# Performance work log

Hardware: AMD Instinct MI355X
Metric: run time of the kernel (lower is better)

## Reference

```python
import jax, jax.numpy as jnp
import numpy as np

N = 50000
E = 1600000
F_IN = 128
F_OUT = 64
NEG_SLOPE = 0.2


def setup_inputs() -> dict:
    key = jax.random.key(0)
    k1, k2, k3, k4, k5, k6 = jax.random.split(key, 6)
    x = jax.random.normal(k1, (N, F_IN), dtype=jnp.float32)
    edge_index = jax.random.randint(k2, (2, E), 0, N, dtype=jnp.int64)
    # GATConv params (heads=1): glorot-ish scale
    W = jax.random.normal(k3, (F_IN, F_OUT), dtype=jnp.float32) * (1.0 / np.sqrt(F_IN))
    att_src = jax.random.normal(k4, (F_OUT,), dtype=jnp.float32) * (1.0 / np.sqrt(F_OUT))
    att_dst = jax.random.normal(k5, (F_OUT,), dtype=jnp.float32) * (1.0 / np.sqrt(F_OUT))
    bias = jnp.zeros((F_OUT,), dtype=jnp.float32)
    return {"x": x, "edge_index": edge_index, "W": W, "att_src": att_src, "att_dst": att_dst, "bias": bias}


def _gat_forward(x, edge_index, W, att_src, att_dst, bias):
    n = x.shape[0]
    # add self loops (PyG GATConv default)
    loops = jnp.arange(n, dtype=edge_index.dtype)
    src = jnp.concatenate([edge_index[0], loops])  # [E+N]
    dst = jnp.concatenate([edge_index[1], loops])  # [E+N]

    h = x @ W                                      # [N, F_OUT]
    a_src = h @ att_src                            # [N]
    a_dst = h @ att_dst                            # [N]

    e = a_src[src] + a_dst[dst]                    # [E+N]
    e = jnp.where(e > 0, e, NEG_SLOPE * e)         # LeakyReLU(0.2)

    # softmax over edges grouped by destination node
    e_max = jax.ops.segment_max(e, dst, num_segments=n)     # [N]
    e_exp = jnp.exp(e - e_max[dst])                          # [E+N]
    e_sum = jax.ops.segment_sum(e_exp, dst, num_segments=n)  # [N]
    alpha = e_exp / e_sum[dst]                               # [E+N]

    msg = h[src] * alpha[:, None]                            # [E+N, F_OUT]
    out = jax.ops.segment_sum(msg, dst, num_segments=n)      # [N, F_OUT]
    out = out + bias
    return jax.nn.relu(out)


def reference(x, edge_index, W, att_src, att_dst, bias):
    return _gat_forward(x, edge_index, W, att_src, att_dst, bias)
```

## Files before the change

kernel.cpp:

```cpp
#include <hip/hip_runtime.h>

#define NN 50000
#define NE 1600000
#define NE4 400000
#define FIN 128
#define FOUT 64
#define SLOPE 0.2f

#define NPB  16
#define NBF  3125
#define CAPB 768
#define GBLK 782
#define CHC4 512
#define LW   136

typedef unsigned int u32;
typedef short short8 __attribute__((ext_vector_type(8)));
typedef float f32x4 __attribute__((ext_vector_type(4)));

__device__ __forceinline__ unsigned short f2bf(float f) {
    u32 u = __float_as_uint(f);
    u += 0x7FFFu + ((u >> 16) & 1u);
    return (unsigned short)(u >> 16);
}
__device__ __forceinline__ float bf2f(unsigned short s) {
    return __uint_as_float(((u32)s) << 16);
}

union FusedLds {
    unsigned short Wt[64 * LW];
    struct { int cnt[NBF]; int gb[NBF]; } f;
};

__global__ __launch_bounds__(256) void fused_k(
        const float* __restrict__ x, const float* __restrict__ W,
        const float* __restrict__ att_s, const float* __restrict__ att_d,
        const int* __restrict__ ei, int* __restrict__ fcur,
        u32* __restrict__ fstage, unsigned short* __restrict__ h,
        float* __restrict__ a_src, float* __restrict__ a_dst) {
    __shared__ FusedLds L;
    const int tid = threadIdx.x;

    {
        unsigned short* Wt = L.Wt;
        const int node0 = blockIdx.x * 64;
        for (int i = tid; i < 128 * 16; i += 256) {
            int k = i >> 4, f = (i & 15) * 4;
            float4 w4 = ((const float4*)W)[i];
            Wt[(f + 0) * LW + k] = f2bf(w4.x);
            Wt[(f + 1) * LW + k] = f2bf(w4.y);
            Wt[(f + 2) * LW + k] = f2bf(w4.z);
            Wt[(f + 3) * LW + k] = f2bf(w4.w);
        }
        const int wv = tid >> 6, lane = tid & 63;
        const int q = lane >> 4, mr = lane & 15;
        const int row = node0 + wv * 16 + mr;
        const bool valid = row < NN;
        const float4* x4 = (const float4*)x;

        short8 afr[4];
        #pragma unroll
        for (int ks = 0; ks < 4; ++ks) {
            float4 f0 = make_float4(0.f, 0.f, 0.f, 0.f), f1 = f0;
            if (valid) {
                f0 = x4[(size_t)row * 32 + ks * 8 + q * 2];
                f1 = x4[(size_t)row * 32 + ks * 8 + q * 2 + 1];
            }
            short8 a;
            a[0] = (short)f2bf(f0.x); a[1] = (short)f2bf(f0.y);
            a[2] = (short)f2bf(f0.z); a[3] = (short)f2bf(f0.w);
            a[4] = (short)f2bf(f1.x); a[5] = (short)f2bf(f1.y);
            a[6] = (short)f2bf(f1.z); a[7] = (short)f2bf(f1.w);
            afr[ks] = a;
        }
        __syncthreads();

        f32x4 acc[4] = {{0,0,0,0},{0,0,0,0},{0,0,0,0},{0,0,0,0}};
        #pragma unroll
        for (int ks = 0; ks < 4; ++ks) {
            #pragma unroll
            for (int nt = 0; nt < 4; ++nt) {
                short8 b = *(const short8*)(Wt + (nt * 16 + mr) * LW + ks * 32 + q * 8);
                acc[nt] = __builtin_amdgcn_mfma_f32_16x16x32_bf16(afr[ks], b, acc[nt], 0, 0, 0);
            }
        }
        float atts[4], attd[4];
        #pragma unroll
        for (int nt = 0; nt < 4; ++nt) {
            atts[nt] = att_s[nt * 16 + mr];
            attd[nt] = att_d[nt * 16 + mr];
        }
        #pragma unroll
        for (int r = 0; r < 4; ++r) {
            int node = node0 + wv * 16 + q * 4 + r;
            float ps = 0.f, pd = 0.f;
            #pragma unroll
            for (int nt = 0; nt < 4; ++nt) {
                float v = acc[nt][r];
                if (node < NN) h[(size_t)node * 64 + nt * 16 + mr] = f2bf(v);
                ps += v * atts[nt];
                pd += v * attd[nt];
            }
            #pragma unroll
            for (int off = 8; off > 0; off >>= 1) {
                ps += __shfl_xor(ps, off);
                pd += __shfl_xor(pd, off);
            }
            if (mr == 0 && node < NN) { a_src[node] = ps; a_dst[node] = pd; }
        }
    }
    __syncthreads();

    for (int i = tid; i < NBF; i += 256) L.f.cnt[i] = 0;
    __syncthreads();

    const int4* sd4 = (const int4*)(ei + NE);
    const int4* ss4 = (const int4*)ei;
    const int lo = blockIdx.x * CHC4;
    int bkx[2][4];
    u32 payx[2][4];
    #pragma unroll
    for (int u = 0; u < 2; ++u) {
        const int i = lo + tid + u * 256;
        if (i < NE4) {
            int4 d = sd4[i];
            int4 s = ss4[i];
            bkx[u][0] = d.x >> 4; payx[u][0] = (u32)s.x | ((u32)(d.x & 15) << 16);
            bkx[u][1] = d.y >> 4; payx[u][1] = (u32)s.y | ((u32)(d.y & 15) << 16);
            bkx[u][2] = d.z >> 4; payx[u][2] = (u32)s.z | ((u32)(d.z & 15) << 16);
            bkx[u][3] = d.w >> 4; payx[u][3] = (u32)s.w | ((u32)(d.w & 15) << 16);
            atomicAdd(&L.f.cnt[bkx[u][0]], 1);
            atomicAdd(&L.f.cnt[bkx[u][1]], 1);
            atomicAdd(&L.f.cnt[bkx[u][2]], 1);
            atomicAdd(&L.f.cnt[bkx[u][3]], 1);
        } else {
            bkx[u][0] = bkx[u][1] = bkx[u][2] = bkx[u][3] = -1;
        }
    }
    __syncthreads();
    for (int b = tid; b < NBF; b += 256) {
        int tot = L.f.cnt[b];
        L.f.gb[b] = tot ? atomicAdd(&fcur[b], tot) : 0;
        L.f.cnt[b] = 0;
    }
    __syncthreads();
    #pragma unroll
    for (int u = 0; u < 2; ++u) {
        #pragma unroll
        for (int e = 0; e < 4; ++e) {
            int b = bkx[u][e];
            if (b >= 0) {
                int pos = L.f.gb[b] + atomicAdd(&L.f.cnt[b], 1);
                if (pos < CAPB) fstage[(size_t)b * CAPB + pos] = payx[u][e];
            }
        }
    }
}

__global__ __launch_bounds__(256) void agg_k(
        const u32* __restrict__ staging, const int* __restrict__ bcur,
        const float* __restrict__ a_src, const float* __restrict__ a_dst,
        const ushort4* __restrict__ h4, const float* __restrict__ bias,
        float* __restrict__ out) {
    const int bkt = blockIdx.x;
    const int node0 = bkt << 4;
    const int nNodes = min(NPB, NN - node0);
    const int bsize = min(bcur[bkt], CAPB);
    const u32* stg = staging + (size_t)bkt * CAPB;
    const int tid = threadIdx.x, wv = tid >> 6, lane = tid & 63;

    __shared__ u32 pk[CAPB];
    __shared__ unsigned short ssrc[CAPB];
    __shared__ int lcnt[NPB];
    __shared__ int lbase[NPB + 1];
    __shared__ int lcur[NPB];
    float* evals = (float*)pk;

    for (int j = tid; j < bsize; j += 256) pk[j] = stg[j];
    if (tid < NPB) lcnt[tid] = 0;
    __syncthreads();
    for (int j = tid; j < bsize; j += 256)
        atomicAdd(&lcnt[pk[j] >> 16], 1);
    __syncthreads();
    if (tid < 64) {
        int v = (tid < NPB) ? lcnt[tid] : 0;
        #pragma unroll
        for (int off = 1; off < NPB; off <<= 1) {
            int u = __shfl_up(v, off);
            if (tid >= off) v += u;
        }
        if (tid < NPB) lbase[tid + 1] = v;
        if (tid == 0) lbase[0] = 0;
    }
    if (tid >= 64 && tid < 64 + NPB) lcur[tid - 64] = 0;
    __syncthreads();
    for (int j = tid; j < bsize; j += 256) {
        u32 w = pk[j];
        int ld = w >> 16;
        int pos = lbase[ld] + atomicAdd(&lcur[ld], 1);
        ssrc[pos] = (unsigned short)(w & 0xFFFFu);
    }
    __syncthreads();

    const int q = lane >> 4, ql = lane & 15;
    const float4 b4 = ((const float4*)bias)[ql];
    const int ln = wv * 4 + q;
    if (ln >= nNodes) return;
    const int n = node0 + ln;
    const int st = lbase[ln], deg = lbase[ln + 1] - st;
    const float ad = a_dst[n];
    float es = a_src[n] + ad; es = es > 0.f ? es : SLOPE * es;
    const float ps = __expf(es);
    float sum = 0.f;
    for (int j = ql; j < deg; j += 16) {
        int s = ssrc[st + j];
        float e = a_src[s] + ad; e = e > 0.f ? e : SLOPE * e;
        float pe = __expf(e);
        evals[st + j] = pe;
        sum += pe;
    }
    sum += __shfl_xor(sum, 8); sum += __shfl_xor(sum, 4);
    sum += __shfl_xor(sum, 2); sum += __shfl_xor(sum, 1);
    const float inv = 1.f / (sum + ps);

    ushort4 hs = h4[(size_t)n * 16 + ql];
    float a0 = ps * bf2f(hs.x), a1 = ps * bf2f(hs.y);
    float a2 = ps * bf2f(hs.z), a3 = ps * bf2f(hs.w);
    int j = 0;
    for (; j + 4 <= deg; j += 4) {
        int s0 = ssrc[st + j], s1 = ssrc[st + j + 1];
        int s2 = ssrc[st + j + 2], s3 = ssrc[st + j + 3];
        float e0 = evals[st + j], e1 = evals[st + j + 1];
        float e2 = evals[st + j + 2], e3 = evals[st + j + 3];
        ushort4 v0 = h4[(size_t)s0 * 16 + ql];
        ushort4 v1 = h4[(size_t)s1 * 16 + ql];
        ushort4 v2 = h4[(size_t)s2 * 16 + ql];
        ushort4 v3 = h4[(size_t)s3 * 16 + ql];
        a0 += e0 * bf2f(v0.x); a1 += e0 * bf2f(v0.y);
        a2 += e0 * bf2f(v0.z); a3 += e0 * bf2f(v0.w);
        a0 += e1 * bf2f(v1.x); a1 += e1 * bf2f(v1.y);
        a2 += e1 * bf2f(v1.z); a3 += e1 * bf2f(v1.w);
        a0 += e2 * bf2f(v2.x); a1 += e2 * bf2f(v2.y);
        a2 += e2 * bf2f(v2.z); a3 += e2 * bf2f(v2.w);
        a0 += e3 * bf2f(v3.x); a1 += e3 * bf2f(v3.y);
        a2 += e3 * bf2f(v3.z); a3 += e3 * bf2f(v3.w);
    }
    for (; j < deg; ++j) {
        int s = ssrc[st + j];
        float ev = evals[st + j];
        ushort4 hv = h4[(size_t)s * 16 + ql];
        a0 += ev * bf2f(hv.x); a1 += ev * bf2f(hv.y);
        a2 += ev * bf2f(hv.z); a3 += ev * bf2f(hv.w);
    }
    float4 o;
    o.x = a0 * inv + b4.x; o.x = o.x > 0.f ? o.x : 0.f;
    o.y = a1 * inv + b4.y; o.y = o.y > 0.f ? o.y : 0.f;
    o.z = a2 * inv + b4.z; o.z = o.z > 0.f ? o.z : 0.f;
    o.w = a3 * inv + b4.w; o.w = o.w > 0.f ? o.w : 0.f;
    ((float4*)out)[(size_t)n * 16 + ql] = o;
}

extern "C" void kernel_launch(void* const* d_in, const int* in_sizes, int n_in,
                              void* d_out, int out_size, void* d_ws, size_t ws_size,
                              hipStream_t stream) {
    const float* x     = (const float*)d_in[0];
    const int*   ei    = (const int*)d_in[1];
    const float* W     = (const float*)d_in[2];
    const float* att_s = (const float*)d_in[3];
    const float* att_d = (const float*)d_in[4];
    const float* bias  = (const float*)d_in[5];
    float* out = (float*)d_out;

    unsigned short* h = (unsigned short*)d_ws;
    float* a_src  = (float*)(h + (size_t)NN * 64);
    float* a_dst  = a_src + NN;
    int*   fcur   = (int*)(a_dst + NN);
    u32*   fstage = (u32*)(fcur + 3200);

    hipMemsetAsync(fcur, 0, NBF * sizeof(int), stream);

    fused_k<<<GBLK, 256, 0, stream>>>(x, W, att_s, att_d, ei, fcur,
                                      fstage, h, a_src, a_dst);
    agg_k<<<NBF, 256, 0, stream>>>(fstage, fcur, a_src, a_dst,
                                   (const ushort4*)h, bias, out);
}
```

Baseline: 169.2 us.

## Coarsen destination buckets to 128 nodes with 1024-thread aggregation blocks

Changes edge binning from 16-node buckets to 128-node buckets, cutting bucket count from 3125 to 391, and runs the aggregation with 1024-thread blocks in which each 16-lane group handles two nodes. The aim is fewer global atomics and smaller LDS counter arrays in the binning pass, and lower block scheduling overhead. The local scan becomes a two-wave scan with a fix-up step. In exchange, aggregation has far fewer blocks, which risks poorer load balance and less latency hiding across CUs.

```diff
diff --git a/kernel.cpp b/kernel.cpp
--- a/kernel.cpp
+++ b/kernel.cpp
@@ -7,9 +7,9 @@
 #define FOUT 64
 #define SLOPE 0.2f
 
-#define NPB  16
-#define NBF  3125
-#define CAPB 768
+#define NPB  128
+#define NBC  391
+#define CAPB 4800
 #define GBLK 782
 #define CHC4 512
 #define LW   136
@@ -29,7 +29,7 @@
 
 union FusedLds {
     unsigned short Wt[64 * LW];
-    struct { int cnt[NBF]; int gb[NBF]; } f;
+    struct { int cnt[NBC]; int gb[NBC]; } f;
 };
 
 __global__ __launch_bounds__(256) void fused_k(
@@ -111,7 +111,7 @@
     }
     __syncthreads();
 
-    for (int i = tid; i < NBF; i += 256) L.f.cnt[i] = 0;
+    for (int i = tid; i < NBC; i += 256) L.f.cnt[i] = 0;
     __syncthreads();
 
     const int4* sd4 = (const int4*)(ei + NE);
@@ -125,10 +125,10 @@
         if (i < NE4) {
             int4 d = sd4[i];
             int4 s = ss4[i];
-            bkx[u][0] = d.x >> 4; payx[u][0] = (u32)s.x | ((u32)(d.x & 15) << 16);
-            bkx[u][1] = d.y >> 4; payx[u][1] = (u32)s.y | ((u32)(d.y & 15) << 16);
-            bkx[u][2] = d.z >> 4; payx[u][2] = (u32)s.z | ((u32)(d.z & 15) << 16);
-            bkx[u][3] = d.w >> 4; payx[u][3] = (u32)s.w | ((u32)(d.w & 15) << 16);
+            bkx[u][0] = d.x >> 7; payx[u][0] = (u32)s.x | ((u32)(d.x & 127) << 16);
+            bkx[u][1] = d.y >> 7; payx[u][1] = (u32)s.y | ((u32)(d.y & 127) << 16);
+            bkx[u][2] = d.z >> 7; payx[u][2] = (u32)s.z | ((u32)(d.z & 127) << 16);
+            bkx[u][3] = d.w >> 7; payx[u][3] = (u32)s.w | ((u32)(d.w & 127) << 16);
             atomicAdd(&L.f.cnt[bkx[u][0]], 1);
             atomicAdd(&L.f.cnt[bkx[u][1]], 1);
             atomicAdd(&L.f.cnt[bkx[u][2]], 1);
@@ -138,7 +138,7 @@
         }
     }
     __syncthreads();
-    for (int b = tid; b < NBF; b += 256) {
+    for (int b = tid; b < NBC; b += 256) {
         int tot = L.f.cnt[b];
         L.f.gb[b] = tot ? atomicAdd(&fcur[b], tot) : 0;
         L.f.cnt[b] = 0;
@@ -157,13 +157,13 @@
     }
 }
 
-__global__ __launch_bounds__(256) void agg_k(
+__global__ __launch_bounds__(1024) void agg_k(
         const u32* __restrict__ staging, const int* __restrict__ bcur,
         const float* __restrict__ a_src, const float* __restrict__ a_dst,
         const ushort4* __restrict__ h4, const float* __restrict__ bias,
         float* __restrict__ out) {
     const int bkt = blockIdx.x;
-    const int node0 = bkt << 4;
+    const int node0 = bkt << 7;
     const int nNodes = min(NPB, NN - node0);
     const int bsize = min(bcur[bkt], CAPB);
     const u32* stg = staging + (size_t)bkt * CAPB;
@@ -176,25 +176,28 @@
     __shared__ int lcur[NPB];
     float* evals = (float*)pk;
 
-    for (int j = tid; j < bsize; j += 256) pk[j] = stg[j];
+    for (int j = tid; j < bsize; j += 1024) pk[j] = stg[j];
     if (tid < NPB) lcnt[tid] = 0;
     __syncthreads();
-    for (int j = tid; j < bsize; j += 256)
+    for (int j = tid; j < bsize; j += 1024)
         atomicAdd(&lcnt[pk[j] >> 16], 1);
     __syncthreads();
-    if (tid < 64) {
-        int v = (tid < NPB) ? lcnt[tid] : 0;
-        #pragma unroll
-        for (int off = 1; off < NPB; off <<= 1) {
+    if (tid < 128) {
+        int l = tid & 63;
+        int v = lcnt[tid];
+        #pragma unroll
+        for (int off = 1; off < 64; off <<= 1) {
             int u = __shfl_up(v, off);
-            if (tid >= off) v += u;
-        }
-        if (tid < NPB) lbase[tid + 1] = v;
+            if (l >= off) v += u;
+        }
+        lbase[tid + 1] = v;
         if (tid == 0) lbase[0] = 0;
     }
-    if (tid >= 64 && tid < 64 + NPB) lcur[tid - 64] = 0;
-    __syncthreads();
-    for (int j = tid; j < bsize; j += 256) {
+    if (tid >= 128 && tid < 256) lcur[tid - 128] = 0;
+    __syncthreads();
+    if (tid >= 64 && tid < 128) lbase[tid + 1] += lbase[64];
+    __syncthreads();
+    for (int j = tid; j < bsize; j += 1024) {
         u32 w = pk[j];
         int ld = w >> 16;
         int pos = lbase[ld] + atomicAdd(&lcur[ld], 1);
@@ -204,60 +207,64 @@
 
     const int q = lane >> 4, ql = lane & 15;
     const float4 b4 = ((const float4*)bias)[ql];
-    const int ln = wv * 4 + q;
-    if (ln >= nNodes) return;
-    const int n = node0 + ln;
-    const int st = lbase[ln], deg = lbase[ln + 1] - st;
-    const float ad = a_dst[n];
-    float es = a_src[n] + ad; es = es > 0.f ? es : SLOPE * es;
-    const float ps = __expf(es);
-    float sum = 0.f;
-    for (int j = ql; j < deg; j += 16) {
-        int s = ssrc[st + j];
-        float e = a_src[s] + ad; e = e > 0.f ? e : SLOPE * e;
-        float pe = __expf(e);
-        evals[st + j] = pe;
-        sum += pe;
-    }
-    sum += __shfl_xor(sum, 8); sum += __shfl_xor(sum, 4);
-    sum += __shfl_xor(sum, 2); sum += __shfl_xor(sum, 1);
-    const float inv = 1.f / (sum + ps);
-
-    ushort4 hs = h4[(size_t)n * 16 + ql];
-    float a0 = ps * bf2f(hs.x), a1 = ps * bf2f(hs.y);
-    float a2 = ps * bf2f(hs.z), a3 = ps * bf2f(hs.w);
-    int j = 0;
-    for (; j + 4 <= deg; j += 4) {
-        int s0 = ssrc[st + j], s1 = ssrc[st + j + 1];
-        int s2 = ssrc[st + j + 2], s3 = ssrc[st + j + 3];
-        float e0 = evals[st + j], e1 = evals[st + j + 1];
-        float e2 = evals[st + j + 2], e3 = evals[st + j + 3];
-        ushort4 v0 = h4[(size_t)s0 * 16 + ql];
-        ushort4 v1 = h4[(size_t)s1 * 16 + ql];
-        ushort4 v2 = h4[(size_t)s2 * 16 + ql];
-        ushort4 v3 = h4[(size_t)s3 * 16 + ql];
-        a0 += e0 * bf2f(v0.x); a1 += e0 * bf2f(v0.y);
-        a2 += e0 * bf2f(v0.z); a3 += e0 * bf2f(v0.w);
-        a0 += e1 * bf2f(v1.x); a1 += e1 * bf2f(v1.y);
-        a2 += e1 * bf2f(v1.z); a3 += e1 * bf2f(v1.w);
-        a0 += e2 * bf2f(v2.x); a1 += e2 * bf2f(v2.y);
-        a2 += e2 * bf2f(v2.z); a3 += e2 * bf2f(v2.w);
-        a0 += e3 * bf2f(v3.x); a1 += e3 * bf2f(v3.y);
-        a2 += e3 * bf2f(v3.z); a3 += e3 * bf2f(v3.w);
-    }
-    for (; j < deg; ++j) {
-        int s = ssrc[st + j];
-        float ev = evals[st + j];
-        ushort4 hv = h4[(size_t)s * 16 + ql];
-        a0 += ev * bf2f(hv.x); a1 += ev * bf2f(hv.y);
-        a2 += ev * bf2f(hv.z); a3 += ev * bf2f(hv.w);
-    }
-    float4 o;
-    o.x = a0 * inv + b4.x; o.x = o.x > 0.f ? o.x : 0.f;
-    o.y = a1 * inv + b4.y; o.y = o.y > 0.f ? o.y : 0.f;
-    o.z = a2 * inv + b4.z; o.z = o.z > 0.f ? o.z : 0.f;
-    o.w = a3 * inv + b4.w; o.w = o.w > 0.f ? o.w : 0.f;
-    ((float4*)out)[(size_t)n * 16 + ql] = o;
+    const int quad = wv * 4 + q;
+    #pragma unroll
+    for (int t = 0; t < 2; ++t) {
+        const int ln = quad * 2 + t;
+        if (ln >= nNodes) continue;
+        const int n = node0 + ln;
+        const int st = lbase[ln], deg = lbase[ln + 1] - st;
+        const float ad = a_dst[n];
+        float es = a_src[n] + ad; es = es > 0.f ? es : SLOPE * es;
+        const float ps = __expf(es);
+        float sum = 0.f;
+        for (int j = ql; j < deg; j += 16) {
+            int s = ssrc[st + j];
+            float e = a_src[s] + ad; e = e > 0.f ? e : SLOPE * e;
+            float pe = __expf(e);
+            evals[st + j] = pe;
+            sum += pe;
+        }
+        sum += __shfl_xor(sum, 8); sum += __shfl_xor(sum, 4);
+        sum += __shfl_xor(sum, 2); sum += __shfl_xor(sum, 1);
+        const float inv = 1.f / (sum + ps);
+
+        ushort4 hs = h4[(size_t)n * 16 + ql];
+        float a0 = ps * bf2f(hs.x), a1 = ps * bf2f(hs.y);
+        float a2 = ps * bf2f(hs.z), a3 = ps * bf2f(hs.w);
+        int j = 0;
+        for (; j + 4 <= deg; j += 4) {
+            int s0 = ssrc[st + j], s1 = ssrc[st + j + 1];
+            int s2 = ssrc[st + j + 2], s3 = ssrc[st + j + 3];
+            float e0 = evals[st + j], e1 = evals[st + j + 1];
+            float e2 = evals[st + j + 2], e3 = evals[st + j + 3];
+            ushort4 v0 = h4[(size_t)s0 * 16 + ql];
+            ushort4 v1 = h4[(size_t)s1 * 16 + ql];
+            ushort4 v2 = h4[(size_t)s2 * 16 + ql];
+            ushort4 v3 = h4[(size_t)s3 * 16 + ql];
+            a0 += e0 * bf2f(v0.x); a1 += e0 * bf2f(v0.y);
+            a2 += e0 * bf2f(v0.z); a3 += e0 * bf2f(v0.w);
+            a0 += e1 * bf2f(v1.x); a1 += e1 * bf2f(v1.y);
+            a2 += e1 * bf2f(v1.z); a3 += e1 * bf2f(v1.w);
+            a0 += e2 * bf2f(v2.x); a1 += e2 * bf2f(v2.y);
+            a2 += e2 * bf2f(v2.z); a3 += e2 * bf2f(v2.w);
+            a0 += e3 * bf2f(v3.x); a1 += e3 * bf2f(v3.y);
+            a2 += e3 * bf2f(v3.z); a3 += e3 * bf2f(v3.w);
+        }
+        for (; j < deg; ++j) {
+            int s = ssrc[st + j];
+            float ev = evals[st + j];
+            ushort4 hv = h4[(size_t)s * 16 + ql];
+            a0 += ev * bf2f(hv.x); a1 += ev * bf2f(hv.y);
+            a2 += ev * bf2f(hv.z); a3 += ev * bf2f(hv.w);
+        }
+        float4 o;
+        o.x = a0 * inv + b4.x; o.x = o.x > 0.f ? o.x : 0.f;
+        o.y = a1 * inv + b4.y; o.y = o.y > 0.f ? o.y : 0.f;
+        o.z = a2 * inv + b4.z; o.z = o.z > 0.f ? o.z : 0.f;
+        o.w = a3 * inv + b4.w; o.w = o.w > 0.f ? o.w : 0.f;
+        ((float4*)out)[(size_t)n * 16 + ql] = o;
+    }
 }
 
 extern "C" void kernel_launch(void* const* d_in, const int* in_sizes, int n_in,
@@ -275,12 +282,12 @@
     float* a_src  = (float*)(h + (size_t)NN * 64);
     float* a_dst  = a_src + NN;
     int*   fcur   = (int*)(a_dst + NN);
-    u32*   fstage = (u32*)(fcur + 3200);
-
-    hipMemsetAsync(fcur, 0, NBF * sizeof(int), stream);
+    u32*   fstage = (u32*)(fcur + 512);
+
+    hipMemsetAsync(fcur, 0, NBC * sizeof(int), stream);
 
     fused_k<<<GBLK, 256, 0, stream>>>(x, W, att_s, att_d, ei, fcur,
                                       fstage, h, a_src, a_dst);
-    agg_k<<<NBF, 256, 0, stream>>>(fstage, fcur, a_src, a_dst,
-                                   (const ushort4*)h, bias, out);
-}
+    agg_k<<<NBC, 1024, 0, stream>>>(fstage, fcur, a_src, a_dst,
+                                    (const ushort4*)h, bias, out);
+}
```

Result: faster. 154.2 us (-8.8%).
